# Optimization experiments

Hardware: AMD Instinct MI355X
Metric: run time of the kernel (lower is better)

## Reference

```python
import jax, jax.numpy as jnp
import numpy as np

SCALE = 0.08838834764831845  # 1/sqrt(head_dim=128)

T, H, D = 8192, 16, 128
NUM_SLOTS = 16384
SEQ_LEN = 2048


def setup_inputs() -> dict:
    key = jax.random.key(0)
    kq, kk, kv = jax.random.split(key, 3)
    q = jax.random.normal(kq, (T, H, D), dtype=jnp.float32)
    k = jax.random.normal(kk, (T, H, D), dtype=jnp.float32)
    v = jax.random.normal(kv, (T, H, D), dtype=jnp.float32)
    k_cache = jnp.zeros((NUM_SLOTS, H * D), dtype=jnp.float32)
    v_cache = jnp.zeros((NUM_SLOTS, H * D), dtype=jnp.float32)
    slot_mapping = jnp.arange(T, dtype=jnp.int32)  # contiguous slots; -1 would mean skip
    return {"q": q, "k": k, "v": v, "k_cache": k_cache, "v_cache": v_cache,
            "slot_mapping": slot_mapping, "seq_len": SEQ_LEN}


def reference(q, k, v, k_cache, v_cache, slot_mapping, seq_len):
    # --- store_kvcache: scatter per-token K/V rows into paged cache slots ---
    t, h, d = q.shape
    num_slots = k_cache.shape[0]
    # slot == -1 means "do not store"; remap to an out-of-bounds index and drop.
    safe_slots = jnp.where(slot_mapping < 0, num_slots, slot_mapping)
    k_cache = k_cache.at[safe_slots].set(k.reshape(t, h * d), mode="drop")
    v_cache = v_cache.at[safe_slots].set(v.reshape(t, h * d), mode="drop")

    # --- prefill attention reading K/V from the cache (block_tables path) ---
    # cu_seqlens = [0, S, 2S, ...]: equal-length sequences packed contiguously,
    # so the per-sequence cache slices are the first t rows reshaped to [B,S,H,D].
    b = t // seq_len
    qb = q.reshape(b, seq_len, h, d)
    kb = k_cache[:t].reshape(b, seq_len, h, d)
    vb = v_cache[:t].reshape(b, seq_len, h, d)

    scores = jnp.einsum("bqhd,bkhd->bhqk", qb, kb) * SCALE  # [B,H,S,S]
    causal = jnp.tril(jnp.ones((seq_len, seq_len), dtype=bool))
    scores = jnp.where(causal[None, None], scores, -jnp.inf)
    p = jax.nn.softmax(scores, axis=-1)
    o = jnp.einsum("bhqk,bkhd->bqhd", p, vb)
    return o.reshape(t, h, d)
```

## Files before the change

kernel.cpp:

```cpp
#include <hip/hip_runtime.h>

typedef float f32x16 __attribute__((ext_vector_type(16)));
typedef __bf16 bf16x8 __attribute__((ext_vector_type(8)));
typedef unsigned int uint2v __attribute__((ext_vector_type(2)));

#define Hh 16
#define Dd 128
#define SEQ 2048
#define HD 2048
#define ATT_C 0.12751743f
#define NEGINF (-__builtin_inff())

__device__ __forceinline__ ushort f2bf(float f) {
    uint u = __builtin_bit_cast(uint, f);
    return (ushort)((u + 0x7FFFu + ((u >> 16) & 1u)) >> 16);
}

__device__ __forceinline__ uint4 pack8(float4 a, float4 b) {
    uint4 u;
    u.x = (uint)f2bf(a.x) | ((uint)f2bf(a.y) << 16);
    u.y = (uint)f2bf(a.z) | ((uint)f2bf(a.w) << 16);
    u.z = (uint)f2bf(b.x) | ((uint)f2bf(b.y) << 16);
    u.w = (uint)f2bf(b.z) | ((uint)f2bf(b.w) << 16);
    return u;
}

__device__ __forceinline__ uint cvtpk(float a, float b) {
    uint r;
    asm("v_cvt_pk_bf16_f32 %0, %1, %2" : "=v"(r) : "v"(a), "v"(b));
    return r;
}

__device__ __forceinline__ f32x16 zero16() {
    f32x16 v;
#pragma unroll
    for (int i = 0; i < 16; ++i) v[i] = 0.f;
    return v;
}

__device__ __forceinline__ void gll16(const void* g, void* l) {
    __builtin_amdgcn_global_load_lds(
        (const __attribute__((address_space(1))) unsigned int*)g,
        (__attribute__((address_space(3))) unsigned int*)l, 16, 0, 0);
}

__device__ __forceinline__ bf16x8 mkfrag(uint a01, uint a23, uint a45, uint a67, int hi) {
    uint4 u;
#if __has_builtin(__builtin_amdgcn_permlane32_swap)
    uint2v xz = __builtin_amdgcn_permlane32_swap(a01, a45, false, false);
    uint2v yw = __builtin_amdgcn_permlane32_swap(a23, a67, false, false);
    u.x = xz[0]; u.y = yw[0]; u.z = xz[1]; u.w = yw[1];
    (void)hi;
#else
    uint s01 = __shfl_xor(a01, 32), s23 = __shfl_xor(a23, 32);
    uint s45 = __shfl_xor(a45, 32), s67 = __shfl_xor(a67, 32);
    u.x = hi ? s45 : a01;
    u.y = hi ? s67 : a23;
    u.z = hi ? a45 : s01;
    u.w = hi ? a67 : s23;
#endif
    return __builtin_bit_cast(bf16x8, u);
}

__global__ void buildinv(const int* __restrict__ slots, int* __restrict__ inv, int T) {
    int t = blockIdx.x * 256 + threadIdx.x;
    if (t < T) { int s = slots[t]; if (s >= 0 && s < T) inv[s] = t; }
}

__global__ void fusekv(const float* __restrict__ k, const float* __restrict__ v,
                       const float* __restrict__ kc, const float* __restrict__ vc,
                       const int* __restrict__ inv, ushort* __restrict__ ek,
                       ushort* __restrict__ evt) {
    __shared__ int sv[64];
    __shared__ ushort Ks[64][136];
    __shared__ ushort Lt[128][72];
    const int tid = threadIdx.x;
    const int r0 = blockIdx.x * 64, h = blockIdx.y;
    const int b = r0 >> 11, tok0 = r0 & (SEQ - 1);
    const long tb = ((long)(b * Hh + h) * 32 + (tok0 >> 6)) * 8192;
    if (tid < 64) sv[tid] = inv[r0 + tid];
    __syncthreads();
#pragma unroll
    for (int i = 0; i < 4; ++i) {
        int idx = i * 256 + tid, r = idx >> 4, sg = idx & 15;
        int s = sv[r];
        const float* src = (s >= 0 ? k + (long)s * HD : kc + (long)(r0 + r) * HD) + h * Dd + sg * 8;
        float4 A = *(const float4*)src;
        float4 Bv = *(const float4*)(src + 4);
        *(uint4*)&Ks[r][sg * 8] = pack8(A, Bv);
    }
    const int d = tid & 127, hf2 = tid >> 7;
#pragma unroll
    for (int i = 0; i < 8; ++i) {
        const int t = i * 8 + hf2 * 4;
        ushort wv[4];
#pragma unroll
        for (int jj = 0; jj < 4; ++jj) {
            int s = sv[t + jj];
            const float* sp = (s >= 0 ? v + (long)s * HD : vc + (long)(r0 + t + jj) * HD) + h * Dd + d;
            wv[jj] = f2bf(*sp);
        }
        uint2 u;
        u.x = (uint)wv[0] | ((uint)wv[1] << 16);
        u.y = (uint)wv[2] | ((uint)wv[3] << 16);
        *(uint2*)&Lt[d][t] = u;
    }
    __syncthreads();
#pragma unroll
    for (int i = 0; i < 4; ++i) {
        int c = i * 256 + tid, l = c & 31, j = (c >> 5) & 15, hf = c >> 9;
        *(uint4*)(ek + tb + (long)c * 8) = *(const uint4*)&Ks[hf * 32 + l][j * 8];
    }
#pragma unroll
    for (int i = 0; i < 4; ++i) {
        int c = i * 256 + tid, l = c & 31, ch = (c >> 5) & 7, nt = c >> 8;
        *(uint4*)(evt + tb + (long)c * 8) = *(const uint4*)&Lt[nt * 32 + l][ch * 8];
    }
}

__global__ __launch_bounds__(512) void attn32(const float* __restrict__ q,
                                              const ushort* __restrict__ ek,
                                              const ushort* __restrict__ evt,
                                              float* __restrict__ out) {
    __shared__ ushort KV[2][16384];

    const int tid = threadIdx.x;
    const int w = tid >> 6, lane = tid & 63;
    const int l31 = lane & 31, hi = lane >> 5;
    const int g = blockIdx.x;
    const int bh = g & 63;
    const int u = g >> 6;
    const int jj = (u < 4) ? u : 11 - u;
    const int b = bh >> 4, h = bh & 15;
    const int ns = 4 * (jj + 1);
    const long kvbase = (long)bh * 32 * 8192;
    const int koff = hi * 256 + l31 * 8;
    const int qtb = jj * 256 + w * 32;
    const int qpos = qtb + l31;

    bf16x8 qf[8];
    {
        const float* qp = q + ((long)(b * SEQ + qtb + l31) * Hh + h) * Dd + hi * 8;
#pragma unroll
        for (int kk = 0; kk < 8; ++kk) {
            float4 A = *(const float4*)(qp + kk * 16);
            float4 Bv = *(const float4*)(qp + kk * 16 + 4);
            A.x *= ATT_C; A.y *= ATT_C; A.z *= ATT_C; A.w *= ATT_C;
            Bv.x *= ATT_C; Bv.y *= ATT_C; Bv.z *= ATT_C; Bv.w *= ATT_C;
            union { uint4 u; bf16x8 v; } cv;
            cv.u = pack8(A, Bv);
            qf[kk] = cv.v;
        }
    }
    auto stage = [&](int nb, int t) {
        const ushort* kg = ek + kvbase + (long)t * 8192 + tid * 8;
        const ushort* vg = evt + kvbase + (long)t * 8192 + tid * 8;
        ushort* kl = &KV[nb][tid * 8];
        ushort* vl = &KV[nb][8192 + tid * 8];
#pragma unroll
        for (int i = 0; i < 2; ++i) {
            gll16(kg + i * 4096, kl + i * 4096);
            gll16(vg + i * 4096, vl + i * 4096);
        }
    };

    f32x16 o[4];
#pragma unroll
    for (int nt = 0; nt < 4; ++nt) o[nt] = zero16();
    float m = NEGINF, lsum = 0.f;

    stage(0, 0);
    __syncthreads();

    int cur = 0;
    for (int s = 0; s < ns; ++s) {
        if (s + 1 < ns) stage(cur ^ 1, s + 1);
        const int kv0 = s * 64;
        const ushort* Kb = &KV[cur][0];
        const ushort* Vb = &KV[cur][8192];

        if (kv0 <= qtb + 31) {
            const bool h2full = (kv0 + 32 <= qtb + 31);
            f32x16 s0 = zero16(), s1;
            __builtin_amdgcn_s_setprio(1);
            if (h2full) {
                s1 = zero16();
#pragma unroll
                for (int kk = 0; kk < 8; ++kk) {
                    s0 = __builtin_amdgcn_mfma_f32_32x32x16_bf16(
                        *(const bf16x8*)&Kb[kk * 512 + koff], qf[kk], s0, 0, 0, 0);
                    s1 = __builtin_amdgcn_mfma_f32_32x32x16_bf16(
                        *(const bf16x8*)&Kb[4096 + kk * 512 + koff], qf[kk], s1, 0, 0, 0);
                }
            } else {
#pragma unroll
                for (int kk = 0; kk < 8; ++kk)
                    s0 = __builtin_amdgcn_mfma_f32_32x32x16_bf16(
                        *(const bf16x8*)&Kb[kk * 512 + koff], qf[kk], s0, 0, 0, 0);
            }
            __builtin_amdgcn_s_setprio(0);

            float mt = NEGINF;
            const bool needmask = (kv0 + 63 > qtb);
            if (needmask) {
#pragma unroll
                for (int r = 0; r < 16; ++r) {
                    const int kr = kv0 + ((r & 3) + 8 * (r >> 2) + 4 * hi);
                    float a0 = (kr <= qpos) ? s0[r] : NEGINF;
                    s0[r] = a0;
                    mt = fmaxf(mt, a0);
                }
                if (h2full) {
#pragma unroll
                    for (int r = 0; r < 16; ++r) {
                        const int kr = kv0 + 32 + ((r & 3) + 8 * (r >> 2) + 4 * hi);
                        float a1 = (kr <= qpos) ? s1[r] : NEGINF;
                        s1[r] = a1;
                        mt = fmaxf(mt, a1);
                    }
                }
            } else {
#pragma unroll
                for (int r = 0; r < 16; ++r) mt = fmaxf(mt, fmaxf(s0[r], s1[r]));
            }
            mt = fmaxf(mt, __shfl_xor(mt, 32));

            if (!__all(mt <= m + 8.f)) {
                const float mn = fmaxf(m, mt);
                const float al = exp2f(m - mn);
                m = mn;
                lsum *= al;
#pragma unroll
                for (int r = 0; r < 16; ++r) {
                    const float alr = __shfl(al, (r & 3) + 8 * (r >> 2) + 4 * hi);
                    o[0][r] *= alr; o[1][r] *= alr; o[2][r] *= alr; o[3][r] *= alr;
                }
            }

            float psum = 0.f;
#pragma unroll
            for (int r = 0; r < 16; ++r) {
                s0[r] = __builtin_amdgcn_exp2f(s0[r] - m);
                psum += s0[r];
            }
            if (h2full) {
#pragma unroll
                for (int r = 0; r < 16; ++r) {
                    s1[r] = __builtin_amdgcn_exp2f(s1[r] - m);
                    psum += s1[r];
                }
            }
            lsum += psum;

            bf16x8 pa00 = mkfrag(cvtpk(s0[0], s0[1]), cvtpk(s0[2], s0[3]),
                                 cvtpk(s0[4], s0[5]), cvtpk(s0[6], s0[7]), hi);
            bf16x8 pa01 = mkfrag(cvtpk(s0[8], s0[9]), cvtpk(s0[10], s0[11]),
                                 cvtpk(s0[12], s0[13]), cvtpk(s0[14], s0[15]), hi);
            __builtin_amdgcn_s_setprio(1);
#pragma unroll
            for (int nt = 0; nt < 4; ++nt) {
                const int vb = nt * 2048 + koff;
                o[nt] = __builtin_amdgcn_mfma_f32_32x32x16_bf16(
                    pa00, *(const bf16x8*)&Vb[vb], o[nt], 0, 0, 0);
                o[nt] = __builtin_amdgcn_mfma_f32_32x32x16_bf16(
                    pa01, *(const bf16x8*)&Vb[vb + 512], o[nt], 0, 0, 0);
            }
            __builtin_amdgcn_s_setprio(0);
            if (h2full) {
                bf16x8 pa10 = mkfrag(cvtpk(s1[0], s1[1]), cvtpk(s1[2], s1[3]),
                                     cvtpk(s1[4], s1[5]), cvtpk(s1[6], s1[7]), hi);
                bf16x8 pa11 = mkfrag(cvtpk(s1[8], s1[9]), cvtpk(s1[10], s1[11]),
                                     cvtpk(s1[12], s1[13]), cvtpk(s1[14], s1[15]), hi);
                __builtin_amdgcn_s_setprio(1);
#pragma unroll
                for (int nt = 0; nt < 4; ++nt) {
                    const int vb = nt * 2048 + koff;
                    o[nt] = __builtin_amdgcn_mfma_f32_32x32x16_bf16(
                        pa10, *(const bf16x8*)&Vb[vb + 1024], o[nt], 0, 0, 0);
                    o[nt] = __builtin_amdgcn_mfma_f32_32x32x16_bf16(
                        pa11, *(const bf16x8*)&Vb[vb + 1536], o[nt], 0, 0, 0);
                }
                __builtin_amdgcn_s_setprio(0);
            }
        }

        __syncthreads();
        cur ^= 1;
    }

    const float lt = lsum + __shfl_xor(lsum, 32);
    const float inv_ = 1.f / lt;
#pragma unroll
    for (int r = 0; r < 16; ++r) {
        const int qr = (r & 3) + 8 * (r >> 2) + 4 * hi;
        const float ivr = __shfl(inv_, qr);
        float* op = out + ((long)(b * SEQ + qtb + qr) * Hh + h) * Dd + l31;
        op[0]  = o[0][r] * ivr;
        op[32] = o[1][r] * ivr;
        op[64] = o[2][r] * ivr;
        op[96] = o[3][r] * ivr;
    }
}

extern "C" void kernel_launch(void* const* d_in, const int* in_sizes, int n_in,
                              void* d_out, int out_size, void* d_ws, size_t ws_size,
                              hipStream_t stream) {
    const float* q = (const float*)d_in[0];
    const float* k = (const float*)d_in[1];
    const float* v = (const float*)d_in[2];
    const float* k_cache = (const float*)d_in[3];
    const float* v_cache = (const float*)d_in[4];
    const int* slot_mapping = (const int*)d_in[5];
    float* out = (float*)d_out;

    const int T = in_sizes[0] / HD;
    (void)n_in; (void)out_size; (void)ws_size;

    ushort* ek = (ushort*)d_ws;
    ushort* evt = ek + (size_t)T * HD;
    int* inv = (int*)(evt + (size_t)T * HD);

    hipMemsetAsync(inv, 0xFF, (size_t)T * sizeof(int), stream);
    buildinv<<<T / 256, 256, 0, stream>>>(slot_mapping, inv, T);
    fusekv<<<dim3(T / 64, Hh), 256, 0, stream>>>(k, v, k_cache, v_cache, inv, ek, evt);
    attn32<<<dim3(512), 512, 0, stream>>>(q, ek, evt, out);
}
```

Measured before the change: 151.2 us.

## Process each 32-key half sequentially with split-accumulator QK and heaviest-first scheduling

New measurement: 150.1 us. About the same (-0.7%).

```diff
diff --git a/kernel.cpp b/kernel.cpp
--- a/kernel.cpp
+++ b/kernel.cpp
@@ -36,6 +36,22 @@
 #pragma unroll
     for (int i = 0; i < 16; ++i) v[i] = 0.f;
     return v;
+}
+
+__device__ __forceinline__ float hsum16(const f32x16 v) {
+    float a0 = v[0] + v[1], a1 = v[2] + v[3], a2 = v[4] + v[5], a3 = v[6] + v[7];
+    float a4 = v[8] + v[9], a5 = v[10] + v[11], a6 = v[12] + v[13], a7 = v[14] + v[15];
+    float b0 = a0 + a1, b1 = a2 + a3, b2 = a4 + a5, b3 = a6 + a7;
+    return (b0 + b1) + (b2 + b3);
+}
+
+__device__ __forceinline__ float hmax16_3(const f32x16 v) {
+    float t0 = fmaxf(fmaxf(v[0], v[1]), v[2]);
+    float t1 = fmaxf(fmaxf(v[3], v[4]), v[5]);
+    float t2 = fmaxf(fmaxf(v[6], v[7]), v[8]);
+    float t3 = fmaxf(fmaxf(v[9], v[10]), v[11]);
+    float t4 = fmaxf(fmaxf(v[12], v[13]), v[14]);
+    return fmaxf(fmaxf(t0, t1), fmaxf(fmaxf(t2, t3), fmaxf(t4, v[15])));
 }
 
 __device__ __forceinline__ void gll16(const void* g, void* l) {
@@ -118,6 +134,57 @@
     }
 }
 
+#define DOHALF(HH)                                                                         \
+  {                                                                                        \
+    f32x16 za = zero16(), zb = zero16();                                                   \
+    __builtin_amdgcn_s_setprio(1);                                                         \
+    _Pragma("unroll")                                                                      \
+    for (int kk = 0; kk < 4; ++kk) {                                                       \
+      za = __builtin_amdgcn_mfma_f32_32x32x16_bf16(                                        \
+          *(const bf16x8*)&Kb[(HH) * 4096 + kk * 512 + koff], qf[kk], za, 0, 0, 0);        \
+      zb = __builtin_amdgcn_mfma_f32_32x32x16_bf16(                                        \
+          *(const bf16x8*)&Kb[(HH) * 4096 + (kk + 4) * 512 + koff], qf[kk + 4], zb, 0, 0, 0); \
+    }                                                                                      \
+    __builtin_amdgcn_s_setprio(0);                                                         \
+    f32x16 z = za + zb;                                                                    \
+    const int kb0 = kv0 + (HH) * 32;                                                       \
+    if (kb0 + 31 > qtb) {                                                                  \
+      _Pragma("unroll")                                                                    \
+      for (int r = 0; r < 16; ++r) {                                                       \
+        const int kr = kb0 + ((r & 3) + 8 * (r >> 2) + 4 * hi);                            \
+        z[r] = (kr <= qpos) ? z[r] : NEGINF;                                               \
+      }                                                                                    \
+    }                                                                                      \
+    float mt = hmax16_3(z);                                                                \
+    mt = fmaxf(mt, __shfl_xor(mt, 32));                                                    \
+    if (!__all(mt <= m + 8.f)) {                                                           \
+      const float mn = fmaxf(m, mt);                                                       \
+      const float al = exp2f(m - mn);                                                      \
+      m = mn;                                                                              \
+      lsum *= al;                                                                          \
+      _Pragma("unroll")                                                                    \
+      for (int r = 0; r < 16; ++r) {                                                       \
+        const float alr = __shfl(al, (r & 3) + 8 * (r >> 2) + 4 * hi);                     \
+        o[0][r] *= alr; o[1][r] *= alr; o[2][r] *= alr; o[3][r] *= alr;                    \
+      }                                                                                    \
+    }                                                                                      \
+    _Pragma("unroll")                                                                      \
+    for (int r = 0; r < 16; ++r) z[r] = __builtin_amdgcn_exp2f(z[r] - m);                  \
+    lsum += hsum16(z);                                                                     \
+    bf16x8 pa0 = mkfrag(cvtpk(z[0], z[1]), cvtpk(z[2], z[3]),                              \
+                        cvtpk(z[4], z[5]), cvtpk(z[6], z[7]), hi);                         \
+    bf16x8 pa1 = mkfrag(cvtpk(z[8], z[9]), cvtpk(z[10], z[11]),                            \
+                        cvtpk(z[12], z[13]), cvtpk(z[14], z[15]), hi);                     \
+    __builtin_amdgcn_s_setprio(1);                                                         \
+    _Pragma("unroll")                                                                      \
+    for (int nt = 0; nt < 4; ++nt) {                                                       \
+      const int vb = nt * 2048 + koff + (HH) * 1024;                                       \
+      o[nt] = __builtin_amdgcn_mfma_f32_32x32x16_bf16(pa0, *(const bf16x8*)&Vb[vb], o[nt], 0, 0, 0);       \
+      o[nt] = __builtin_amdgcn_mfma_f32_32x32x16_bf16(pa1, *(const bf16x8*)&Vb[vb + 512], o[nt], 0, 0, 0); \
+    }                                                                                      \
+    __builtin_amdgcn_s_setprio(0);                                                         \
+  }
+
 __global__ __launch_bounds__(512) void attn32(const float* __restrict__ q,
                                               const ushort* __restrict__ ek,
                                               const ushort* __restrict__ evt,
@@ -129,8 +196,7 @@
     const int l31 = lane & 31, hi = lane >> 5;
     const int g = blockIdx.x;
     const int bh = g & 63;
-    const int u = g >> 6;
-    const int jj = (u < 4) ? u : 11 - u;
+    const int jj = 7 - (g >> 6);
     const int b = bh >> 4, h = bh & 15;
     const int ns = 4 * (jj + 1);
     const long kvbase = (long)bh * 32 * 8192;
@@ -180,108 +246,8 @@
         const ushort* Vb = &KV[cur][8192];
 
         if (kv0 <= qtb + 31) {
-            const bool h2full = (kv0 + 32 <= qtb + 31);
-            f32x16 s0 = zero16(), s1;
-            __builtin_amdgcn_s_setprio(1);
-            if (h2full) {
-                s1 = zero16();
-#pragma unroll
-                for (int kk = 0; kk < 8; ++kk) {
-                    s0 = __builtin_amdgcn_mfma_f32_32x32x16_bf16(
-                        *(const bf16x8*)&Kb[kk * 512 + koff], qf[kk], s0, 0, 0, 0);
-                    s1 = __builtin_amdgcn_mfma_f32_32x32x16_bf16(
-                        *(const bf16x8*)&Kb[4096 + kk * 512 + koff], qf[kk], s1, 0, 0, 0);
-                }
-            } else {
-#pragma unroll
-                for (int kk = 0; kk < 8; ++kk)
-                    s0 = __builtin_amdgcn_mfma_f32_32x32x16_bf16(
-                        *(const bf16x8*)&Kb[kk * 512 + koff], qf[kk], s0, 0, 0, 0);
-            }
-            __builtin_amdgcn_s_setprio(0);
-
-            float mt = NEGINF;
-            const bool needmask = (kv0 + 63 > qtb);
-            if (needmask) {
-#pragma unroll
-                for (int r = 0; r < 16; ++r) {
-                    const int kr = kv0 + ((r & 3) + 8 * (r >> 2) + 4 * hi);
-                    float a0 = (kr <= qpos) ? s0[r] : NEGINF;
-                    s0[r] = a0;
-                    mt = fmaxf(mt, a0);
-                }
-                if (h2full) {
-#pragma unroll
-                    for (int r = 0; r < 16; ++r) {
-                        const int kr = kv0 + 32 + ((r & 3) + 8 * (r >> 2) + 4 * hi);
-                        float a1 = (kr <= qpos) ? s1[r] : NEGINF;
-                        s1[r] = a1;
-                        mt = fmaxf(mt, a1);
-                    }
-                }
-            } else {
-#pragma unroll
-                for (int r = 0; r < 16; ++r) mt = fmaxf(mt, fmaxf(s0[r], s1[r]));
-            }
-            mt = fmaxf(mt, __shfl_xor(mt, 32));
-
-            if (!__all(mt <= m + 8.f)) {
-                const float mn = fmaxf(m, mt);
-                const float al = exp2f(m - mn);
-                m = mn;
-                lsum *= al;
-#pragma unroll
-                for (int r = 0; r < 16; ++r) {
-                    const float alr = __shfl(al, (r & 3) + 8 * (r >> 2) + 4 * hi);
-                    o[0][r] *= alr; o[1][r] *= alr; o[2][r] *= alr; o[3][r] *= alr;
-                }
-            }
-
-            float psum = 0.f;
-#pragma unroll
-            for (int r = 0; r < 16; ++r) {
-                s0[r] = __builtin_amdgcn_exp2f(s0[r] - m);
-                psum += s0[r];
-            }
-            if (h2full) {
-#pragma unroll
-                for (int r = 0; r < 16; ++r) {
-                    s1[r] = __builtin_amdgcn_exp2f(s1[r] - m);
-                    psum += s1[r];
-                }
-            }
-            lsum += psum;
-
-            bf16x8 pa00 = mkfrag(cvtpk(s0[0], s0[1]), cvtpk(s0[2], s0[3]),
-                                 cvtpk(s0[4], s0[5]), cvtpk(s0[6], s0[7]), hi);
-            bf16x8 pa01 = mkfrag(cvtpk(s0[8], s0[9]), cvtpk(s0[10], s0[11]),
-                                 cvtpk(s0[12], s0[13]), cvtpk(s0[14], s0[15]), hi);
-            __builtin_amdgcn_s_setprio(1);
-#pragma unroll
-            for (int nt = 0; nt < 4; ++nt) {
-                const int vb = nt * 2048 + koff;
-                o[nt] = __builtin_amdgcn_mfma_f32_32x32x16_bf16(
-                    pa00, *(const bf16x8*)&Vb[vb], o[nt], 0, 0, 0);
-                o[nt] = __builtin_amdgcn_mfma_f32_32x32x16_bf16(
-                    pa01, *(const bf16x8*)&Vb[vb + 512], o[nt], 0, 0, 0);
-            }
-            __builtin_amdgcn_s_setprio(0);
-            if (h2full) {
-                bf16x8 pa10 = mkfrag(cvtpk(s1[0], s1[1]), cvtpk(s1[2], s1[3]),
-                                     cvtpk(s1[4], s1[5]), cvtpk(s1[6], s1[7]), hi);
-                bf16x8 pa11 = mkfrag(cvtpk(s1[8], s1[9]), cvtpk(s1[10], s1[11]),
-                                     cvtpk(s1[12], s1[13]), cvtpk(s1[14], s1[15]), hi);
-                __builtin_amdgcn_s_setprio(1);
-#pragma unroll
-                for (int nt = 0; nt < 4; ++nt) {
-                    const int vb = nt * 2048 + koff;
-                    o[nt] = __builtin_amdgcn_mfma_f32_32x32x16_bf16(
-                        pa10, *(const bf16x8*)&Vb[vb + 1024], o[nt], 0, 0, 0);
-                    o[nt] = __builtin_amdgcn_mfma_f32_32x32x16_bf16(
-                        pa11, *(const bf16x8*)&Vb[vb + 1536], o[nt], 0, 0, 0);
-                }
-                __builtin_amdgcn_s_setprio(0);
-            }
+            DOHALF(0);
+            if (kv0 + 32 <= qtb + 31) DOHALF(1);
         }
 
         __syncthreads();
```
